# Performance work log

Measured on AMD Instinct MI355X. Metric: run time of the kernel, lower is better.

Reference implementation:

```python
import jax, jax.numpy as jnp
import numpy as np

D_MODEL = 2048
NUM_HEADS = 16
D_KV = D_MODEL // NUM_HEADS
THETA = 10000.0
N_LORA = 4
RANK = 16
BATCH = 2
SEQ = 2048


def setup_inputs() -> dict:
    key = jax.random.key(0)
    ks = jax.random.split(key, 16)
    s = 0.02
    inp = {
        'x': jax.random.normal(ks[0], (BATCH, SEQ, D_MODEL), jnp.float32),
        'lora_start_indices': jnp.sort(jax.random.randint(ks[1], (N_LORA,), 0, BATCH)),
        'Wq': jax.random.normal(ks[2], (D_MODEL, D_MODEL), jnp.float32) * s,
        'Aq': jax.random.normal(ks[3], (N_LORA, RANK, D_MODEL), jnp.float32) * s,
        'Bq': jax.random.normal(ks[4], (N_LORA, D_MODEL, RANK), jnp.float32) * s,
        'Wk': jax.random.normal(ks[5], (D_MODEL, D_MODEL), jnp.float32) * s,
        'Ak': jax.random.normal(ks[6], (N_LORA, RANK, D_MODEL), jnp.float32) * s,
        'Bk': jax.random.normal(ks[7], (N_LORA, D_MODEL, RANK), jnp.float32) * s,
        'Wv': jax.random.normal(ks[8], (D_MODEL, D_MODEL), jnp.float32) * s,
        'Av': jax.random.normal(ks[9], (N_LORA, RANK, D_MODEL), jnp.float32) * s,
        'Bv': jax.random.normal(ks[10], (N_LORA, D_MODEL, RANK), jnp.float32) * s,
        'Wo': jax.random.normal(ks[11], (D_MODEL, D_MODEL), jnp.float32) * s,
        'Ao': jax.random.normal(ks[12], (N_LORA, RANK, D_MODEL), jnp.float32) * s,
        'Bo': jax.random.normal(ks[13], (N_LORA, D_MODEL, RANK), jnp.float32) * s,
    }
    return inp


def _adapter_ids(starts, batch):
    # each batch row b uses the adapter whose start index is the last one <= b
    ids = jnp.searchsorted(starts, jnp.arange(batch), side='right') - 1
    return jnp.clip(ids, 0, starts.shape[0] - 1)


def _multilora(x, ids, W, A, B):
    # x: [b, s, d_in]; W: [d_out, d_in]; A: [L, r, d_in]; B: [L, d_out, r]
    base = jnp.einsum('bsd,od->bso', x, W)
    Ai, Bi = A[ids], B[ids]                       # [b, r, d_in], [b, d_out, r]
    low = jnp.einsum('bsd,brd->bsr', x, Ai)
    return base + jnp.einsum('bsr,bor->bso', low, Bi)


def _rope(x):
    # x: [b, h, s, d]; interleaved pair rotation
    d = x.shape[-1]
    pos = jnp.arange(x.shape[-2], dtype=jnp.float32)
    inv_freq = THETA ** (-jnp.arange(0, d, 2, dtype=jnp.float32) / d)  # [d/2]
    ang = pos[:, None] * inv_freq[None, :]                              # [s, d/2]
    cos, sin = jnp.cos(ang), jnp.sin(ang)
    x1, x2 = x[..., 0::2], x[..., 1::2]
    o1 = x1 * cos - x2 * sin
    o2 = x1 * sin + x2 * cos
    return jnp.stack([o1, o2], axis=-1).reshape(x.shape)


def reference(x, lora_start_indices, Wq, Aq, Bq, Wk, Ak, Bk, Wv, Av, Bv, Wo, Ao, Bo):
    b, s, _ = x.shape
    ids = _adapter_ids(lora_start_indices, b)
    Q = _multilora(x, ids, Wq, Aq, Bq)
    K = _multilora(x, ids, Wk, Ak, Bk)
    V = _multilora(x, ids, Wv, Av, Bv)
    # [b, s, h*d] -> [b, h, s, d]
    split = lambda t: t.reshape(b, s, NUM_HEADS, D_KV).transpose(0, 2, 1, 3)
    Q, K, V = split(Q), split(K), split(V)
    Q, K = _rope(Q), _rope(K)
    scores = jnp.einsum('bhqd,bhkd->bhqk', Q, K) / jnp.sqrt(jnp.asarray(D_KV, x.dtype))
    causal = jnp.tril(jnp.ones((s, s), bool))
    scores = jnp.where(causal, scores, jnp.asarray(-jnp.inf, scores.dtype))
    attn = jax.nn.softmax(scores, axis=-1)
    out = jnp.einsum('bhqk,bhkd->bhqd', attn, V)
    out = out.transpose(0, 2, 1, 3).reshape(b, s, D_MODEL)
    return _multilora(out, ids, Wo, Ao, Bo)
```

## Files before the change

### kernel.cpp

```cpp
#include <hip/hip_runtime.h>

typedef unsigned short u16;
typedef unsigned int   u32;
typedef __bf16  bf16x8 __attribute__((ext_vector_type(8)));
typedef float   f32x4  __attribute__((ext_vector_type(4)));

#define D_MODEL 2048
#define SEQ     2048
#define NHEAD   16
#define DKV     128
#define RANK    16

__device__ __forceinline__ u16 f2b(float f) {
  union { float f; u32 i; } v; v.f = f;
  u32 i = v.i;
  return (u16)((i + 0x7FFFu + ((i >> 16) & 1u)) >> 16);
}
__device__ __forceinline__ u32 pack2(float lo, float hi) {
  return (u32)f2b(lo) | ((u32)f2b(hi) << 16);
}
__device__ __forceinline__ float b2f(u16 u) {
  union { u32 i; float f; } v; v.i = ((u32)u) << 16; return v.f;
}
__device__ __forceinline__ float dot2(u32 xa, u32 aa) {
  return b2f((u16)(xa & 0xFFFFu)) * b2f((u16)(aa & 0xFFFFu)) +
         b2f((u16)(xa >> 16))     * b2f((u16)(aa >> 16));
}
__device__ __forceinline__ int adapter_id(const int* starts, int b) {
  int cnt = 0;
#pragma unroll
  for (int i = 0; i < 4; ++i) cnt += (starts[i] <= b) ? 1 : 0;
  int id = cnt - 1;
  return id < 0 ? 0 : (id > 3 ? 3 : id);
}
__device__ __forceinline__ f32x4 mfma16(bf16x8 a, bf16x8 b, f32x4 c) {
  return __builtin_amdgcn_mfma_f32_16x16x32_bf16(a, b, c, 0, 0, 0);
}

struct CvtArgs {
  const float* src[13];
  u32 base[14];
};
__global__ __launch_bounds__(256) void convert_kernel(CvtArgs a, u16* __restrict__ dst) {
  const u32 c = blockIdx.x * 256 + threadIdx.x;
  const u32 el0 = c * 8;
  if (el0 >= a.base[13]) return;
  int t = 0;
#pragma unroll
  for (int i = 1; i < 13; ++i) t += (el0 >= a.base[i]) ? 1 : 0;
  const float* s = a.src[t] + (el0 - a.base[t]);
  const float4 lo = *(const float4*)s;
  const float4 hi = *(const float4*)(s + 4);
  uint4 r;
  r.x = pack2(lo.x, lo.y); r.y = pack2(lo.z, lo.w);
  r.z = pack2(hi.x, hi.y); r.w = pack2(hi.z, hi.w);
  *(uint4*)(dst + el0) = r;
}

__global__ __launch_bounds__(256) void lowrank_kernel(
    const u16* __restrict__ X, const u16* __restrict__ A0,
    const u16* __restrict__ A1, const u16* __restrict__ A2,
    const int* __restrict__ starts, float* __restrict__ low, int nout)
{
  const int m = blockIdx.x;
  const int w = threadIdx.x >> 6, lane = threadIdx.x & 63;
  const int id = adapter_id(starts, m >> 11);
  const u16* Xr = X + (size_t)m * D_MODEL;
  for (int o = w; o < nout; o += 4) {
    const int p = o >> 4, r = o & 15;
    const u16* Ar = (p == 0 ? A0 : p == 1 ? A1 : A2) + (size_t)(id * 16 + r) * D_MODEL;
    float sum = 0.f;
#pragma unroll
    for (int c = 0; c < 4; ++c) {
      const int d = c * 512 + lane * 8;
      const uint4 xv = *(const uint4*)(Xr + d);
      const uint4 av = *(const uint4*)(Ar + d);
      sum += dot2(xv.x, av.x) + dot2(xv.y, av.y) + dot2(xv.z, av.z) + dot2(xv.w, av.w);
    }
#pragma unroll
    for (int off = 32; off >= 1; off >>= 1) sum += __shfl_xor(sum, off, 64);
    if (lane == 0) low[(size_t)m * nout + o] = sum;
  }
}

__global__ __launch_bounds__(256, 2) void gemm_kernel(
    const u16* __restrict__ X,
    const u16* __restrict__ W0, const u16* __restrict__ W1, const u16* __restrict__ W2,
    const u16* __restrict__ B0, const u16* __restrict__ B1, const u16* __restrict__ B2,
    const float* __restrict__ low, int ldlow,
    const int* __restrict__ starts,
    u16* __restrict__ D0, u16* __restrict__ D1, u16* __restrict__ D2,
    float* __restrict__ Df, int qkv)
{
  __shared__ __attribute__((aligned(16))) u16 At[128 * 32];
  __shared__ __attribute__((aligned(16))) u16 Bt[128 * 32];
  const int tid = threadIdx.x;
  const int w = tid >> 6, lane = tid & 63, quad = lane >> 4, l16 = lane & 15;
  const int wr = w >> 1, wc = w & 1;
  const int n0 = blockIdx.x * 128, m0 = blockIdx.y * 128, z = blockIdx.z;
  const u16* W  = (z == 0) ? W0 : (z == 1) ? W1 : W2;
  const u16* Bm = (z == 0) ? B0 : (z == 1) ? B1 : B2;
  u16*       D  = (z == 0) ? D0 : (z == 1) ? D1 : D2;
  const int loff = qkv ? z * RANK : 0;
  const int id = adapter_id(starts, m0 >> 11);

  const f32x4 zero4 = {0.f, 0.f, 0.f, 0.f};
  f32x4 acc[4][4];
#pragma unroll
  for (int i = 0; i < 4; ++i)
#pragma unroll
    for (int j = 0; j < 4; ++j) acc[i][j] = zero4;

  const int srow = tid >> 2;
  const int scol = (tid & 3) * 8;
  const u16* Xg = X + (size_t)(m0 + srow) * D_MODEL + scol;
  const u16* Wg = W + (size_t)(n0 + srow) * D_MODEL + scol;

  uint4 ra0 = *(const uint4*)(Xg);
  uint4 ra1 = *(const uint4*)(Xg + 64 * D_MODEL);
  uint4 rb0 = *(const uint4*)(Wg);
  uint4 rb1 = *(const uint4*)(Wg + 64 * D_MODEL);

  for (int kt = 0; kt < D_MODEL / 32; ++kt) {
    *(uint4*)(At + srow * 32 + scol)        = ra0;
    *(uint4*)(At + (64 + srow) * 32 + scol) = ra1;
    *(uint4*)(Bt + srow * 32 + scol)        = rb0;
    *(uint4*)(Bt + (64 + srow) * 32 + scol) = rb1;
    __syncthreads();
    if (kt < D_MODEL / 32 - 1) {
      const int kb = (kt + 1) * 32;
      ra0 = *(const uint4*)(Xg + kb);
      ra1 = *(const uint4*)(Xg + 64 * D_MODEL + kb);
      rb0 = *(const uint4*)(Wg + kb);
      rb1 = *(const uint4*)(Wg + 64 * D_MODEL + kb);
    }
    bf16x8 af[4], bfr[4];
#pragma unroll
    for (int i = 0; i < 4; ++i)
      af[i] = *(const bf16x8*)&At[(wr * 64 + i * 16 + l16) * 32 + quad * 8];
#pragma unroll
    for (int j = 0; j < 4; ++j)
      bfr[j] = *(const bf16x8*)&Bt[(wc * 64 + j * 16 + l16) * 32 + quad * 8];
#pragma unroll
    for (int i = 0; i < 4; ++i)
#pragma unroll
      for (int j = 0; j < 4; ++j)
        acc[i][j] = mfma16(af[i], bfr[j], acc[i][j]);
    __syncthreads();
  }

  for (int e = tid; e < 4096; e += 256) {
    const int rr = e >> 5, kk = e & 31;
    u16 av = 0, bv = 0;
    if (kk < RANK) {
      av = f2b(low[(size_t)(m0 + rr) * ldlow + loff + kk]);
      bv = Bm[((size_t)id * D_MODEL + n0 + rr) * RANK + kk];
    }
    At[rr * 32 + kk] = av;
    Bt[rr * 32 + kk] = bv;
  }
  __syncthreads();
  {
    bf16x8 af[4], bfr[4];
#pragma unroll
    for (int i = 0; i < 4; ++i)
      af[i] = *(const bf16x8*)&At[(wr * 64 + i * 16 + l16) * 32 + quad * 8];
#pragma unroll
    for (int j = 0; j < 4; ++j)
      bfr[j] = *(const bf16x8*)&Bt[(wc * 64 + j * 16 + l16) * 32 + quad * 8];
#pragma unroll
    for (int i = 0; i < 4; ++i)
#pragma unroll
      for (int j = 0; j < 4; ++j)
        acc[i][j] = mfma16(af[i], bfr[j], acc[i][j]);
  }

  const float scale = (qkv && z == 0) ? 0.08838834764831845f : 1.0f;
#pragma unroll
  for (int i = 0; i < 4; ++i) {
    const int mrow = m0 + wr * 64 + i * 16 + quad * 4;
#pragma unroll
    for (int j = 0; j < 4; ++j) {
      const int col = n0 + wc * 64 + j * 16 + l16;
#pragma unroll
      for (int r = 0; r < 4; ++r) {
        const float v = acc[i][j][r] * scale;
        const int m = mrow + r;
        if (qkv) {
          const int bb = m >> 11, s = m & (SEQ - 1);
          const int hh = col >> 7, jj = col & (DKV - 1);
          D[(((size_t)(bb * NHEAD + hh)) * SEQ + s) * DKV + jj] = f2b(v);
        } else {
          Df[(size_t)m * D_MODEL + col] = v;
        }
      }
    }
  }
}

__global__ __launch_bounds__(256) void rope_kernel(u16* __restrict__ Q, u16* __restrict__ K) {
  const u32 idx = blockIdx.x * 256 + threadIdx.x;
  u16* T = (idx & 4194304u) ? K : Q;
  const u32 r  = idx & 4194303u;
  const u32 i  = r & 63u;
  const u32 s  = (r >> 6) & 2047u;
  const u32 bh = r >> 17;
  u16* p = T + ((size_t)bh * SEQ + s) * DKV + 2 * i;
  const u32 v = *(const u32*)p;
  const float x1 = b2f((u16)(v & 0xFFFFu)), x2 = b2f((u16)(v >> 16));
  const float ang = (float)s * exp2f(-0.20762050593046f * (float)i);
  float sn, cs;
  __sincosf(ang, &sn, &cs);
  *(u32*)p = pack2(x1 * cs - x2 * sn, x1 * sn + x2 * cs);
}

#define M0 8.0f
__global__ __launch_bounds__(256, 3) void flash_kernel(
    const u16* __restrict__ Q, const u16* __restrict__ K,
    const u16* __restrict__ V, u16* __restrict__ O,
    u16* __restrict__ Opart, float* __restrict__ lpart)
{
  __shared__ __attribute__((aligned(16))) u16 Kl[64 * 136];
  __shared__ __attribute__((aligned(16))) u16 VT[DKV * 72];
  __shared__ __attribute__((aligned(16))) u16 Pl[4 * 16 * 72];
  const int tid = threadIdx.x;
  const int w = tid >> 6, lane = tid & 63, quad = lane >> 4, l16 = lane & 15;
  const int cid = blockIdx.x, bh = blockIdx.y;
  const size_t base = (size_t)bh * SEQ * DKV;
  const u16* Qb = Q + base;
  const u16* Kb = K + base;
  const u16* Vb = V + base;
  const int b = bh >> 4, h = bh & 15;
  u16* Plw = &Pl[w * 1152];
  const f32x4 zero4 = {0.f, 0.f, 0.f, 0.f};

  const int dual = (cid < 16);
  const int nA   = dual ? (cid + 1) : 16;
  const int qtB  = 31 - cid;
  const int n    = dual ? 17 : 16;

  const int krr = tid >> 4;
  const int kc8 = (tid & 15) * 8;
  const int vrp = tid & 31;
  const int vcg = tid >> 5;

  int qt = cid, q0 = cid * 64;
  bf16x8 qa[4];
#pragma unroll
  for (int kc = 0; kc < 4; ++kc)
    qa[kc] = *(const bf16x8*)(Qb + (size_t)(q0 + w * 16 + l16) * DKV + kc * 32 + quad * 8);

  f32x4 oacc[8];
#pragma unroll
  for (int nn = 0; nn < 8; ++nn) oacc[nn] = zero4;
  float lr[4] = {0.f, 0.f, 0.f, 0.f};

  uint4 pk[4], pva[2], pvb[2];
#pragma unroll
  for (int it = 0; it < 4; ++it)
    pk[it] = *(const uint4*)(Kb + (size_t)(krr + it * 16) * DKV + kc8);
#pragma unroll
  for (int it = 0; it < 2; ++it) {
    pva[it] = *(const uint4*)(Vb + (size_t)(2 * vrp)     * DKV + (vcg + it * 8) * 8);
    pvb[it] = *(const uint4*)(Vb + (size_t)(2 * vrp + 1) * DKV + (vcg + it * 8) * 8);
  }

  for (int s = 0; s < n; ++s) {
    if (dual && s == nA) {
      float inv[4];
#pragma unroll
      for (int rg = 0; rg < 4; ++rg) {
        float t = lr[rg];
#pragma unroll
        for (int off = 8; off >= 1; off >>= 1) t += __shfl_xor(t, off, 64);
        inv[rg] = 1.f / t;
        lr[rg] = 0.f;
      }
#pragma unroll
      for (int nn = 0; nn < 8; ++nn) {
        const int col = h * DKV + nn * 16 + l16;
#pragma unroll
        for (int rg = 0; rg < 4; ++rg) {
          const int row = q0 + w * 16 + quad * 4 + rg;
          O[((size_t)b * SEQ + row) * D_MODEL + col] = f2b(oacc[nn][rg] * inv[rg]);
        }
#pragma unroll
        for (int e = 0; e < 4; ++e) oacc[nn][e] = 0.f;
      }
      qt = qtB; q0 = qtB * 64;
#pragma unroll
      for (int kc = 0; kc < 4; ++kc)
        qa[kc] = *(const bf16x8*)(Qb + (size_t)(q0 + w * 16 + l16) * DKV + kc * 32 + quad * 8);
    }
    const int kt = (dual && s >= nA) ? (16 + s - nA) : s;

    __syncthreads();
#pragma unroll
    for (int it = 0; it < 4; ++it)
      *(uint4*)(&Kl[(krr + it * 16) * 136 + kc8]) = pk[it];
#pragma unroll
    for (int it = 0; it < 2; ++it) {
      const int c0 = (vcg + it * 8) * 8;
      const uint4 a = pva[it], c = pvb[it];
      *(u32*)&VT[(c0 + 0) * 72 + 2 * vrp] = (a.x & 0xFFFFu) | (c.x << 16);
      *(u32*)&VT[(c0 + 1) * 72 + 2 * vrp] = (a.x >> 16)     | (c.x & 0xFFFF0000u);
      *(u32*)&VT[(c0 + 2) * 72 + 2 * vrp] = (a.y & 0xFFFFu) | (c.y << 16);
      *(u32*)&VT[(c0 + 3) * 72 + 2 * vrp] = (a.y >> 16)     | (c.y & 0xFFFF0000u);
      *(u32*)&VT[(c0 + 4) * 72 + 2 * vrp] = (a.z & 0xFFFFu) | (c.z << 16);
      *(u32*)&VT[(c0 + 5) * 72 + 2 * vrp] = (a.z >> 16)     | (c.z & 0xFFFF0000u);
      *(u32*)&VT[(c0 + 6) * 72 + 2 * vrp] = (a.w & 0xFFFFu) | (c.w << 16);
      *(u32*)&VT[(c0 + 7) * 72 + 2 * vrp] = (a.w >> 16)     | (c.w & 0xFFFF0000u);
    }
    __syncthreads();

    if (s + 1 < n) {
      const int ktn = (dual && (s + 1) >= nA) ? (16 + s + 1 - nA) : (s + 1);
      const size_t ko = (size_t)ktn * 64 * DKV;
#pragma unroll
      for (int it = 0; it < 4; ++it)
        pk[it] = *(const uint4*)(Kb + ko + (size_t)(krr + it * 16) * DKV + kc8);
#pragma unroll
      for (int it = 0; it < 2; ++it) {
        pva[it] = *(const uint4*)(Vb + ko + (size_t)(2 * vrp)     * DKV + (vcg + it * 8) * 8);
        pvb[it] = *(const uint4*)(Vb + ko + (size_t)(2 * vrp + 1) * DKV + (vcg + it * 8) * 8);
      }
    }

    f32x4 sacc[4];
#pragma unroll
    for (int jc = 0; jc < 4; ++jc) sacc[jc] = zero4;
#pragma unroll
    for (int kc = 0; kc < 4; ++kc)
#pragma unroll
      for (int jc = 0; jc < 4; ++jc) {
        const bf16x8 kb = *(const bf16x8*)&Kl[(jc * 16 + l16) * 136 + kc * 32 + quad * 8];
        sacc[jc] = mfma16(qa[kc], kb, sacc[jc]);
      }

    const int diag = (kt == qt);
#pragma unroll
    for (int rg = 0; rg < 4; ++rg) {
      const int qq = q0 + w * 16 + quad * 4 + rg;
      float psum = 0.f;
#pragma unroll
      for (int jc = 0; jc < 4; ++jc) {
        const int kk = kt * 64 + jc * 16 + l16;
        float p = __expf(sacc[jc][rg] - M0);
        if (diag && kk > qq) p = 0.f;
        psum += p;
        Plw[(quad * 4 + rg) * 72 + jc * 16 + l16] = f2b(p);
      }
      lr[rg] += psum;
    }

#pragma unroll
    for (int kc = 0; kc < 2; ++kc) {
      const bf16x8 pa = *(const bf16x8*)&Plw[l16 * 72 + kc * 32 + quad * 8];
#pragma unroll
      for (int nn = 0; nn < 8; ++nn) {
        const bf16x8 vb = *(const bf16x8*)&VT[(nn * 16 + l16) * 72 + kc * 32 + quad * 8];
        oacc[nn] = mfma16(pa, vb, oacc[nn]);
      }
    }
  }

  const int j = dual ? 1 : 0;
  const int slot = (bh * 16 + (qt - 16)) * 2 + j;
#pragma unroll
  for (int rg = 0; rg < 4; ++rg) {
#pragma unroll
    for (int off = 8; off >= 1; off >>= 1) lr[rg] += __shfl_xor(lr[rg], off, 64);
  }
#pragma unroll
  for (int nn = 0; nn < 8; ++nn) {
#pragma unroll
    for (int rg = 0; rg < 4; ++rg) {
      const int row = w * 16 + quad * 4 + rg;
      Opart[(size_t)slot * 8192 + row * 128 + nn * 16 + l16] = f2b(oacc[nn][rg]);
    }
  }
  if (l16 == 0) {
#pragma unroll
    for (int rg = 0; rg < 4; ++rg)
      lpart[slot * 64 + w * 16 + quad * 4 + rg] = lr[rg];
  }
}

__global__ __launch_bounds__(256) void merge_kernel(
    const u16* __restrict__ Opart, const float* __restrict__ lpart,
    u16* __restrict__ O)
{
  const u32 t = blockIdx.x * 256 + threadIdx.x;
  const u32 u   = t & 63;
  const u32 row = (t >> 6) & 63;
  const u32 q16 = (t >> 12) & 15;
  const u32 bh  = t >> 16;
  const u32 slot0 = (bh * 16 + q16) * 2;
  const u32 o0 = ((slot0 * 8192u + row * 128u) >> 1) + u;
  const u32 a = ((const u32*)Opart)[o0];
  const u32 c = ((const u32*)Opart)[o0 + 4096];
  const float inv = 1.f / (lpart[slot0 * 64 + row] + lpart[(slot0 + 1) * 64 + row]);
  const float r0 = (b2f((u16)(a & 0xFFFFu)) + b2f((u16)(c & 0xFFFFu))) * inv;
  const float r1 = (b2f((u16)(a >> 16))     + b2f((u16)(c >> 16)))     * inv;
  const u32 bb = bh >> 4, h = bh & 15;
  const u32 s = (q16 + 16) * 64 + row;
  ((u32*)O)[(size_t)(bb * SEQ + s) * (D_MODEL / 2) + h * 64 + u] = pack2(r0, r1);
}

extern "C" void kernel_launch(void* const* d_in, const int* in_sizes, int n_in,
                              void* d_out, int out_size, void* d_ws, size_t ws_size,
                              hipStream_t stream) {
  (void)in_sizes; (void)n_in; (void)out_size; (void)ws_size;
  const int* starts = (const int*)d_in[1];

  static const u32 XB = 0;
  static const u32 WQ = 8388608, WK = 12582912, WV = 16777216, WO = 20971520;
  static const u32 AQ = 25165824, AK = 25296896, AV = 25427968, AO = 25559040;
  static const u32 BQ = 25690112, BK = 25821184, BV = 25952256, BO = 26083328;
  static const u32 TOT = 26214400;

  u16* wsb = (u16*)d_ws;
  char* ws = (char*)d_ws;
  float* low_qkv = (float*)(ws + 52428800);
  float* low_o   = (float*)(ws + 53215232);
  u16*   Qb      = (u16*)(ws + 53477376);
  u16*   Kb      = (u16*)(ws + 70254592);
  u16*   Vb      = (u16*)(ws + 87031808);
  u16*   attn    = wsb + XB;
  u16*   Opart   = wsb + WQ;
  float* lpart   = (float*)(ws + 33554432);

  CvtArgs ca;
  ca.src[0]  = (const float*)d_in[0];
  ca.src[1]  = (const float*)d_in[2];
  ca.src[2]  = (const float*)d_in[5];
  ca.src[3]  = (const float*)d_in[8];
  ca.src[4]  = (const float*)d_in[11];
  ca.src[5]  = (const float*)d_in[3];
  ca.src[6]  = (const float*)d_in[6];
  ca.src[7]  = (const float*)d_in[9];
  ca.src[8]  = (const float*)d_in[12];
  ca.src[9]  = (const float*)d_in[4];
  ca.src[10] = (const float*)d_in[7];
  ca.src[11] = (const float*)d_in[10];
  ca.src[12] = (const float*)d_in[13];
  const u32 bases[14] = {XB, WQ, WK, WV, WO, AQ, AK, AV, AO, BQ, BK, BV, BO, TOT};
  for (int i = 0; i < 14; ++i) ca.base[i] = bases[i];

  convert_kernel<<<dim3(TOT / 8 / 256), 256, 0, stream>>>(ca, wsb);

  lowrank_kernel<<<dim3(4096), 256, 0, stream>>>(wsb + XB, wsb + AQ, wsb + AK, wsb + AV,
                                                 starts, low_qkv, 48);
  gemm_kernel<<<dim3(16, 32, 3), 256, 0, stream>>>(
      wsb + XB, wsb + WQ, wsb + WK, wsb + WV, wsb + BQ, wsb + BK, wsb + BV,
      low_qkv, 48, starts, Qb, Kb, Vb, (float*)nullptr, 1);
  rope_kernel<<<dim3(32768), 256, 0, stream>>>(Qb, Kb);
  flash_kernel<<<dim3(32, 32), 256, 0, stream>>>(Qb, Kb, Vb, attn, Opart, lpart);
  merge_kernel<<<dim3(8192), 256, 0, stream>>>(Opart, lpart, attn);
  lowrank_kernel<<<dim3(4096), 256, 0, stream>>>(attn, wsb + AO, wsb + AO, wsb + AO,
                                                 starts, low_o, 16);
  gemm_kernel<<<dim3(16, 32, 1), 256, 0, stream>>>(
      attn, wsb + WO, wsb + WO, wsb + WO, wsb + BO, wsb + BO, wsb + BO,
      low_o, 16, starts, (u16*)nullptr, (u16*)nullptr, (u16*)nullptr,
      (float*)d_out, 0);
}
```

Baseline: 542.9 us.

## Fuse RoPE into QKV GEMM epilogue and template GEMM on QKV mode

The standalone RoPE kernel is removed and the rotation is applied in the QKV GEMM epilogue. Each lane computes sin/cos for its column and swaps the interleaved pair partner with a lane shuffle. The GEMM is templated on QKV mode so the epilogue branch is resolved at compile time. The flash split-partial buffers move into the output buffer, which is overwritten later by the final GEMM. This saves a full read/write pass over Q and K and one launch, at the cost of extra transcendental work in the GEMM epilogue.

Result: faster. 521.6 us (-3.9%).

```diff
diff --git a/kernel.cpp b/kernel.cpp
--- a/kernel.cpp
+++ b/kernel.cpp
@@ -41,7 +41,7 @@
   const float* src[13];
   u32 base[14];
 };
-__global__ __launch_bounds__(256) void convert_kernel(CvtArgs a, u16* __restrict__ dst) {
+__global__ __launch_bounds__(256) void k_convert(CvtArgs a, u16* __restrict__ dst) {
   const u32 c = blockIdx.x * 256 + threadIdx.x;
   const u32 el0 = c * 8;
   if (el0 >= a.base[13]) return;
@@ -57,7 +57,8 @@
   *(uint4*)(dst + el0) = r;
 }
 
-__global__ __launch_bounds__(256) void lowrank_kernel(
+template <int TAG>
+__global__ __launch_bounds__(256) void k_lowrank(
     const u16* __restrict__ X, const u16* __restrict__ A0,
     const u16* __restrict__ A1, const u16* __restrict__ A2,
     const int* __restrict__ starts, float* __restrict__ low, int nout)
@@ -83,14 +84,15 @@
   }
 }
 
-__global__ __launch_bounds__(256, 2) void gemm_kernel(
+template <int QKV>
+__global__ __launch_bounds__(256, 2) void k_gemm(
     const u16* __restrict__ X,
     const u16* __restrict__ W0, const u16* __restrict__ W1, const u16* __restrict__ W2,
     const u16* __restrict__ B0, const u16* __restrict__ B1, const u16* __restrict__ B2,
     const float* __restrict__ low, int ldlow,
     const int* __restrict__ starts,
     u16* __restrict__ D0, u16* __restrict__ D1, u16* __restrict__ D2,
-    float* __restrict__ Df, int qkv)
+    float* __restrict__ Df)
 {
   __shared__ __attribute__((aligned(16))) u16 At[128 * 32];
   __shared__ __attribute__((aligned(16))) u16 Bt[128 * 32];
@@ -101,7 +103,7 @@
   const u16* W  = (z == 0) ? W0 : (z == 1) ? W1 : W2;
   const u16* Bm = (z == 0) ? B0 : (z == 1) ? B1 : B2;
   u16*       D  = (z == 0) ? D0 : (z == 1) ? D1 : D2;
-  const int loff = qkv ? z * RANK : 0;
+  const int loff = QKV ? z * RANK : 0;
   const int id = adapter_id(starts, m0 >> 11);
 
   const f32x4 zero4 = {0.f, 0.f, 0.f, 0.f};
@@ -175,47 +177,49 @@
         acc[i][j] = mfma16(af[i], bfr[j], acc[i][j]);
   }
 
-  const float scale = (qkv && z == 0) ? 0.08838834764831845f : 1.0f;
-#pragma unroll
-  for (int i = 0; i < 4; ++i) {
-    const int mrow = m0 + wr * 64 + i * 16 + quad * 4;
-#pragma unroll
-    for (int j = 0; j < 4; ++j) {
-      const int col = n0 + wc * 64 + j * 16 + l16;
-#pragma unroll
-      for (int r = 0; r < 4; ++r) {
-        const float v = acc[i][j][r] * scale;
-        const int m = mrow + r;
-        if (qkv) {
-          const int bb = m >> 11, s = m & (SEQ - 1);
-          const int hh = col >> 7, jj = col & (DKV - 1);
-          D[(((size_t)(bb * NHEAD + hh)) * SEQ + s) * DKV + jj] = f2b(v);
-        } else {
-          Df[(size_t)m * D_MODEL + col] = v;
+  if (QKV) {
+    const float scale = (z == 0) ? 0.08838834764831845f : 1.0f;
+    const int ropez = (z <= 1);
+#pragma unroll
+    for (int i = 0; i < 4; ++i) {
+      const int mrow = m0 + wr * 64 + i * 16 + quad * 4;
+#pragma unroll
+      for (int j = 0; j < 4; ++j) {
+        const int col = n0 + wc * 64 + j * 16 + l16;
+        const int hh = col >> 7, jj = col & (DKV - 1);
+        const float invf = exp2f(-0.20762050593046f * (float)(jj >> 1));
+#pragma unroll
+        for (int r = 0; r < 4; ++r) {
+          const int m = mrow + r;
+          const int bb = m >> 11, srw = m & (SEQ - 1);
+          float v = acc[i][j][r] * scale;
+          if (ropez) {
+            float sn, cs;
+            __sincosf((float)srw * invf, &sn, &cs);
+            const float part = __shfl_xor(v, 1, 64);
+            v = (jj & 1) ? (part * sn + v * cs) : (v * cs - part * sn);
+          }
+          D[(((size_t)(bb * NHEAD + hh)) * SEQ + srw) * DKV + jj] = f2b(v);
         }
       }
     }
-  }
-}
-
-__global__ __launch_bounds__(256) void rope_kernel(u16* __restrict__ Q, u16* __restrict__ K) {
-  const u32 idx = blockIdx.x * 256 + threadIdx.x;
-  u16* T = (idx & 4194304u) ? K : Q;
-  const u32 r  = idx & 4194303u;
-  const u32 i  = r & 63u;
-  const u32 s  = (r >> 6) & 2047u;
-  const u32 bh = r >> 17;
-  u16* p = T + ((size_t)bh * SEQ + s) * DKV + 2 * i;
-  const u32 v = *(const u32*)p;
-  const float x1 = b2f((u16)(v & 0xFFFFu)), x2 = b2f((u16)(v >> 16));
-  const float ang = (float)s * exp2f(-0.20762050593046f * (float)i);
-  float sn, cs;
-  __sincosf(ang, &sn, &cs);
-  *(u32*)p = pack2(x1 * cs - x2 * sn, x1 * sn + x2 * cs);
+  } else {
+#pragma unroll
+    for (int i = 0; i < 4; ++i) {
+      const int mrow = m0 + wr * 64 + i * 16 + quad * 4;
+#pragma unroll
+      for (int j = 0; j < 4; ++j) {
+        const int col = n0 + wc * 64 + j * 16 + l16;
+#pragma unroll
+        for (int r = 0; r < 4; ++r)
+          Df[(size_t)(mrow + r) * D_MODEL + col] = acc[i][j][r];
+      }
+    }
+  }
 }
 
 #define M0 8.0f
-__global__ __launch_bounds__(256, 3) void flash_kernel(
+__global__ __launch_bounds__(256, 3) void k_flash(
     const u16* __restrict__ Q, const u16* __restrict__ K,
     const u16* __restrict__ V, u16* __restrict__ O,
     u16* __restrict__ Opart, float* __restrict__ lpart)
@@ -386,7 +390,7 @@
   }
 }
 
-__global__ __launch_bounds__(256) void merge_kernel(
+__global__ __launch_bounds__(256) void k_merge(
     const u16* __restrict__ Opart, const float* __restrict__ lpart,
     u16* __restrict__ O)
 {
@@ -427,8 +431,8 @@
   u16*   Kb      = (u16*)(ws + 70254592);
   u16*   Vb      = (u16*)(ws + 87031808);
   u16*   attn    = wsb + XB;
-  u16*   Opart   = wsb + WQ;
-  float* lpart   = (float*)(ws + 33554432);
+  u16*   Opart   = (u16*)d_out;
+  float* lpart   = (float*)((char*)d_out + 16777216);
 
   CvtArgs ca;
   ca.src[0]  = (const float*)d_in[0];
@@ -447,20 +451,19 @@
   const u32 bases[14] = {XB, WQ, WK, WV, WO, AQ, AK, AV, AO, BQ, BK, BV, BO, TOT};
   for (int i = 0; i < 14; ++i) ca.base[i] = bases[i];
 
-  convert_kernel<<<dim3(TOT / 8 / 256), 256, 0, stream>>>(ca, wsb);
-
-  lowrank_kernel<<<dim3(4096), 256, 0, stream>>>(wsb + XB, wsb + AQ, wsb + AK, wsb + AV,
-                                                 starts, low_qkv, 48);
-  gemm_kernel<<<dim3(16, 32, 3), 256, 0, stream>>>(
+  k_convert<<<dim3(TOT / 8 / 256), 256, 0, stream>>>(ca, wsb);
+
+  k_lowrank<0><<<dim3(4096), 256, 0, stream>>>(wsb + XB, wsb + AQ, wsb + AK, wsb + AV,
+                                               starts, low_qkv, 48);
+  k_gemm<1><<<dim3(16, 32, 3), 256, 0, stream>>>(
       wsb + XB, wsb + WQ, wsb + WK, wsb + WV, wsb + BQ, wsb + BK, wsb + BV,
-      low_qkv, 48, starts, Qb, Kb, Vb, (float*)nullptr, 1);
-  rope_kernel<<<dim3(32768), 256, 0, stream>>>(Qb, Kb);
-  flash_kernel<<<dim3(32, 32), 256, 0, stream>>>(Qb, Kb, Vb, attn, Opart, lpart);
-  merge_kernel<<<dim3(8192), 256, 0, stream>>>(Opart, lpart, attn);
-  lowrank_kernel<<<dim3(4096), 256, 0, stream>>>(attn, wsb + AO, wsb + AO, wsb + AO,
-                                                 starts, low_o, 16);
-  gemm_kernel<<<dim3(16, 32, 1), 256, 0, stream>>>(
+      low_qkv, 48, starts, Qb, Kb, Vb, (float*)nullptr);
+  k_flash<<<dim3(32, 32), 256, 0, stream>>>(Qb, Kb, Vb, attn, Opart, lpart);
+  k_merge<<<dim3(8192), 256, 0, stream>>>(Opart, lpart, attn);
+  k_lowrank<1><<<dim3(4096), 256, 0, stream>>>(attn, wsb + AO, wsb + AO, wsb + AO,
+                                               starts, low_o, 16);
+  k_gemm<0><<<dim3(16, 32, 1), 256, 0, stream>>>(
       attn, wsb + WO, wsb + WO, wsb + WO, wsb + BO, wsb + BO, wsb + BO,
       low_o, 16, starts, (u16*)nullptr, (u16*)nullptr, (u16*)nullptr,
-      (float*)d_out, 0);
-}
+      (float*)d_out);
+}
```
